# Kernel optimization log

Measured on AMD Instinct MI355X. Metric: run time of the kernel, lower is better.

## Reference

```python
import jax, jax.numpy as jnp
import numpy as np

MIN_BIN = 3.25
MAX_BIN = 20.75
NUM_BINS = 15
INF = 100000000.0
N = 1536
D_PAIR = 128

def setup_inputs() -> dict:
    key = jax.random.key(0)
    k1, k2, k3 = jax.random.split(key, 3)
    x = jax.random.normal(k1, (N, 3), dtype=jnp.float32)
    W = jax.random.normal(k2, (D_PAIR, NUM_BINS), dtype=jnp.float32)
    b = jax.random.normal(k3, (D_PAIR,), dtype=jnp.float32)
    return {"x": x, "W": W, "b": b}

def reference(x, W, b):
    # squared bin edges, like torch.linspace(min,max,num_bins)**2
    bins = jnp.linspace(MIN_BIN, MAX_BIN, NUM_BINS, dtype=jnp.float32) ** 2  # [num_bins]
    upper = jnp.concatenate([bins[1:], jnp.array([INF], dtype=jnp.float32)])  # [num_bins]
    # pairwise squared distances: [N, N, 1]
    d = jnp.sum((x[:, None, :] - x[None, :, :]) ** 2, axis=-1, keepdims=True)
    # one-hot binning: strictly greater than lower edge, strictly less than upper edge
    oh = ((d > bins) & (d < upper)).astype(W.dtype)  # [N, N, num_bins]
    # linear projection: [N, N, d_pair]
    return jnp.einsum('ijk,pk->ijp', oh, W) + b
```

## Files before the change

### kernel.cpp

```cpp
#include <hip/hip_runtime.h>


#define NBINS 15
#define NPTS  1536
#define DPAIR 128

typedef float f32x4 __attribute__((ext_vector_type(4)));

__global__ __launch_bounds__(256) void recycling_embedder_kernel(
    const float* __restrict__ x,
    const float* __restrict__ W,
    const float* __restrict__ b,
    float* __restrict__ out,
    unsigned total_f4) {
    __shared__ float table[16 * DPAIR];
    __shared__ float xs[NPTS * 3];

    float bins[NBINS];
#pragma unroll
    for (int k = 0; k < NBINS; ++k) {
        float e = 3.25f + 1.25f * (float)k;
        bins[k] = e * e;
    }

    for (int e = threadIdx.x; e < 16 * DPAIR; e += blockDim.x) {
        int idx = e >> 7;
        int p   = e & (DPAIR - 1);
        float v = b[p];
        if (idx > 0) v += W[p * NBINS + (idx - 1)];
        table[e] = v;
    }
    for (int e = threadIdx.x; e < NPTS * 3; e += blockDim.x) xs[e] = x[e];
    __syncthreads();

    const f32x4* table4 = (const f32x4*)table;
    f32x4* out4 = (f32x4*)out;

    unsigned stride = gridDim.x * blockDim.x;
    for (unsigned g = blockIdx.x * blockDim.x + threadIdx.x; g < total_f4; g += stride) {
        unsigned pair   = g >> 5;
        unsigned within = g & 31u;
        unsigned i = pair / NPTS;
        unsigned j = pair - i * NPTS;

        float d;
        {
#pragma clang fp contract(off)
            float dx = xs[i * 3 + 0] - xs[j * 3 + 0];
            float dy = xs[i * 3 + 1] - xs[j * 3 + 1];
            float dz = xs[i * 3 + 2] - xs[j * 3 + 2];
            d = dx * dx + dy * dy + dz * dz;
        }

        int cnt = 0;
        int eq = 0;
#pragma unroll
        for (int k = 0; k < NBINS; ++k) {
            cnt += (d > bins[k]) ? 1 : 0;
            eq  |= (d == bins[k]) ? 1 : 0;
        }
        int idx = eq ? 0 : cnt;

        f32x4 v = table4[idx * (DPAIR / 4) + within];
        __builtin_nontemporal_store(v, out4 + g);
    }
}

extern "C" void kernel_launch(void* const* d_in, const int* in_sizes, int n_in,
                              void* d_out, int out_size, void* d_ws, size_t ws_size,
                              hipStream_t stream) {
    const float* x = (const float*)d_in[0];
    const float* W = (const float*)d_in[1];
    const float* b = (const float*)d_in[2];
    float* out = (float*)d_out;

    const unsigned total_f4 = (unsigned)NPTS * NPTS * (DPAIR / 4);
    dim3 grid(1536), block(256);
    recycling_embedder_kernel<<<grid, block, 0, stream>>>(x, W, b, out, total_f4);
}
```

Measured before the change: 1.208 ms.

## Assign one output row per block and precompute bin indices in LDS

Each block now handles one row i. It computes the 1536 distance bin indices once per j into a byte array in LDS, then streams the row's output by looking them up in the table. This removes the redundant distance and bin computation that used to run for every float4 (32 times per pair), and it drops the 18KB LDS copy of x. It also replaces nontemporal stores with ordinary stores, which may change how write bandwidth behaves on this store-bound kernel.

```diff
diff --git a/kernel.cpp b/kernel.cpp
--- a/kernel.cpp
+++ b/kernel.cpp
@@ -4,6 +4,7 @@
 #define NBINS 15
 #define NPTS  1536
 #define DPAIR 128
+#define ROW_F4 (NPTS * DPAIR / 4)
 
 typedef float f32x4 __attribute__((ext_vector_type(4)));
 
@@ -11,10 +12,12 @@
     const float* __restrict__ x,
     const float* __restrict__ W,
     const float* __restrict__ b,
-    float* __restrict__ out,
-    unsigned total_f4) {
+    float* __restrict__ out) {
     __shared__ float table[16 * DPAIR];
-    __shared__ float xs[NPTS * 3];
+    __shared__ unsigned char idx_lds[NPTS];
+
+    const int i = blockIdx.x;
+    const int t = threadIdx.x;
 
     float bins[NBINS];
 #pragma unroll
@@ -23,46 +26,44 @@
         bins[k] = e * e;
     }
 
-    for (int e = threadIdx.x; e < 16 * DPAIR; e += blockDim.x) {
-        int idx = e >> 7;
+    for (int e = t; e < 16 * DPAIR; e += 256) {
+        int row = e >> 7;
         int p   = e & (DPAIR - 1);
         float v = b[p];
-        if (idx > 0) v += W[p * NBINS + (idx - 1)];
+        if (row > 0) v += W[p * NBINS + (row - 1)];
         table[e] = v;
     }
-    for (int e = threadIdx.x; e < NPTS * 3; e += blockDim.x) xs[e] = x[e];
-    __syncthreads();
 
-    const f32x4* table4 = (const f32x4*)table;
-    f32x4* out4 = (f32x4*)out;
-
-    unsigned stride = gridDim.x * blockDim.x;
-    for (unsigned g = blockIdx.x * blockDim.x + threadIdx.x; g < total_f4; g += stride) {
-        unsigned pair   = g >> 5;
-        unsigned within = g & 31u;
-        unsigned i = pair / NPTS;
-        unsigned j = pair - i * NPTS;
-
+    const float xi0 = x[i * 3 + 0];
+    const float xi1 = x[i * 3 + 1];
+    const float xi2 = x[i * 3 + 2];
+    for (int j = t; j < NPTS; j += 256) {
         float d;
         {
 #pragma clang fp contract(off)
-            float dx = xs[i * 3 + 0] - xs[j * 3 + 0];
-            float dy = xs[i * 3 + 1] - xs[j * 3 + 1];
-            float dz = xs[i * 3 + 2] - xs[j * 3 + 2];
+            float dx = xi0 - x[j * 3 + 0];
+            float dy = xi1 - x[j * 3 + 1];
+            float dz = xi2 - x[j * 3 + 2];
             d = dx * dx + dy * dy + dz * dz;
         }
-
-        int cnt = 0;
-        int eq = 0;
+        int cnt = 0, eq = 0;
 #pragma unroll
         for (int k = 0; k < NBINS; ++k) {
             cnt += (d > bins[k]) ? 1 : 0;
             eq  |= (d == bins[k]) ? 1 : 0;
         }
-        int idx = eq ? 0 : cnt;
+        idx_lds[j] = (unsigned char)(eq ? 0 : cnt);
+    }
+    __syncthreads();
 
-        f32x4 v = table4[idx * (DPAIR / 4) + within];
-        __builtin_nontemporal_store(v, out4 + g);
+    const f32x4* table4 = (const f32x4*)table;
+    f32x4* orow = (f32x4*)out + (size_t)i * ROW_F4;
+#pragma unroll 4
+    for (int l = t; l < ROW_F4; l += 256) {
+        int j      = l >> 5;
+        int within = l & 31;
+        int idx    = idx_lds[j];
+        orow[l] = table4[idx * (DPAIR / 4) + within];
     }
 }
 
@@ -74,7 +75,6 @@
     const float* b = (const float*)d_in[2];
     float* out = (float*)d_out;
 
-    const unsigned total_f4 = (unsigned)NPTS * NPTS * (DPAIR / 4);
-    dim3 grid(1536), block(256);
-    recycling_embedder_kernel<<<grid, block, 0, stream>>>(x, W, b, out, total_f4);
+    dim3 grid(NPTS), block(256);
+    recycling_embedder_kernel<<<grid, block, 0, stream>>>(x, W, b, out);
 }
```

Result: faster. 1.178 ms (-2.5%).
